# Optimization experiments

Hardware: AMD Instinct MI355X
Metric: run time of the kernel (lower is better)

Reference implementation:

```python
import jax, jax.numpy as jnp
import numpy as np

B, H, W, D = 8, 64, 64, 512
NH, DK = 16, 32
WS, SH = 8, 4            # window size, shift size = WS // 2
L = 4                    # n_layer
WS2 = WS * WS
NWH, NWW = H // WS, W // WS
SCALE = 1.0 / np.sqrt(DK)


def _rel_index(ws):
    # standard Swin relative position index: (ws^2, ws^2) into a (2ws-1)^2 table
    coords = np.stack(np.meshgrid(np.arange(ws), np.arange(ws), indexing='ij'))
    cf = coords.reshape(2, -1)
    rel = cf[:, :, None] - cf[:, None, :] + (ws - 1)
    return (rel[0] * (2 * ws - 1) + rel[1]).astype(np.int32)


def _shift_mask():
    # Swin-style shifted-window attention mask for cyclic shift by SH
    img = np.zeros((H, W), dtype=np.int32)
    cnt = 0
    sls = (slice(0, -WS), slice(-WS, -SH), slice(-SH, None))
    for hs in sls:
        for ws_ in sls:
            img[hs, ws_] = cnt
            cnt += 1
    win = img.reshape(NWH, WS, NWW, WS).transpose(0, 2, 1, 3).reshape(NWH, NWW, WS2)
    m = win[..., None, :] != win[..., :, None]          # (nh, nw, ws2, ws2)
    return np.broadcast_to(m[None, None], (1, NH, NWH, NWW, WS2, WS2)).copy()


def setup_inputs() -> dict:
    key = jax.random.key(0)
    ks = jax.random.split(key, 12)
    s = 0.02
    inp = {
        'x': jax.random.normal(ks[0], (B, H, W, D), jnp.float32),
        'mask': jnp.asarray(_shift_mask()),
        'rel_index': jnp.asarray(_rel_index(WS)),
        'Wq': jax.random.normal(ks[1], (L, D, D), jnp.float32) * s,
        'bq': jnp.zeros((L, D), jnp.float32),
        'Wkv': jax.random.normal(ks[2], (L, D, 2 * D), jnp.float32) * s,
        'bkv': jnp.zeros((L, 2 * D), jnp.float32),
        'Wo': jax.random.normal(ks[3], (L, D, D), jnp.float32) * s,
        'bo': jnp.zeros((L, D), jnp.float32),
        'rel_table': jax.random.normal(ks[4], (L, (2 * WS - 1) ** 2, NH), jnp.float32) * s,
        'ln1_g': jnp.ones((L, D), jnp.float32),
        'ln1_b': jnp.zeros((L, D), jnp.float32),
        'ln2_g': jnp.ones((L, D), jnp.float32),
        'ln2_b': jnp.zeros((L, D), jnp.float32),
        'W1': jax.random.normal(ks[5], (L, D, 4 * D), jnp.float32) * s,
        'b1': jnp.zeros((L, 4 * D), jnp.float32),
        'W2': jax.random.normal(ks[6], (L, 4 * D, D), jnp.float32) * s,
        'b2': jnp.zeros((L, D), jnp.float32),
    }
    return inp


def _ln(x, g, b):
    m = jnp.mean(x, -1, keepdims=True)
    v = jnp.mean(jnp.square(x - m), -1, keepdims=True)
    return (x - m) * jax.lax.rsqrt(v + 1e-5) * g + b


def _partition(t):
    # (B,H,W,NH,DK) -> (B,NH,nh,nw,ws^2,DK)
    t = t.reshape(B, NWH, WS, NWW, WS, NH, DK)
    return t.transpose(0, 5, 1, 3, 2, 4, 6).reshape(B, NH, NWH, NWW, WS2, DK)


def _merge(t):
    # (B,NH,nh,nw,ws^2,DK) -> (B,H,W,NH,DK)
    t = t.reshape(B, NH, NWH, NWW, WS, WS, DK).transpose(0, 2, 4, 3, 5, 1, 6)
    return t.reshape(B, H, W, NH, DK)


def _attn(xn, mask, rel_index, Wq, bq, Wkv, bkv, Wo, bo, table):
    q = (xn @ Wq + bq).reshape(B, H, W, NH, DK)
    kv = (xn @ Wkv + bkv).reshape(B, H, W, 2, NH, DK)
    k, v = kv[..., 0, :, :], kv[..., 1, :, :]
    # cyclic shift (shifting=True since n_class=4)
    q = jnp.roll(q, (-SH, -SH), axis=(1, 2))
    k = jnp.roll(k, (-SH, -SH), axis=(1, 2))
    v = jnp.roll(v, (-SH, -SH), axis=(1, 2))
    qw, kw, vw = _partition(q), _partition(k), _partition(v)
    scores = jnp.einsum('bhnmqd,bhnmkd->bhnmqk', qw, kw) * SCALE
    bias = table[rel_index]                      # (ws2, ws2, NH)
    scores = scores + bias.transpose(2, 0, 1)[None, :, None, None]
    scores = jnp.where(mask, -1e9, scores)
    a = jax.nn.softmax(scores, axis=-1)
    o = jnp.einsum('bhnmqk,bhnmkd->bhnmqd', a, vw)
    o = _merge(o)
    o = jnp.roll(o, (SH, SH), axis=(1, 2))       # reverse cyclic shift
    return o.reshape(B, H, W, D) @ Wo + bo


def reference(x, mask, rel_index, Wq, bq, Wkv, bkv, Wo, bo, rel_table,
              ln1_g, ln1_b, ln2_g, ln2_b, W1, b1, W2, b2):
    for i in range(L):
        x = x + _attn(_ln(x, ln1_g[i], ln1_b[i]), mask, rel_index,
                      Wq[i], bq[i], Wkv[i], bkv[i], Wo[i], bo[i], rel_table[i])
        h = _ln(x, ln2_g[i], ln2_b[i])
        x = x + (jax.nn.gelu(h @ W1[i] + b1[i]) @ W2[i] + b2[i])
    return x
```

## Files before the change

### kernel.cpp

```cpp
#include <hip/hip_runtime.h>
#include <hip/hip_bf16.h>

typedef __hip_bfloat16 bf16;
typedef __attribute__((ext_vector_type(8))) short short8;
typedef __attribute__((ext_vector_type(4))) float f32x4;

#define GLDS16(g, l) __builtin_amdgcn_global_load_lds(                              \
    (__attribute__((address_space(1))) const void*)(g),                             \
    (__attribute__((address_space(3))) void*)(l), 16, 0, 0)

#define SCALE_ 0.17677669529663687f

__global__ void detect_k(const unsigned int* __restrict__ ln1g_raw, int* __restrict__ flag)
{
    if (threadIdx.x == 0) *flag = (ln1g_raw[0] == 0x3F803F80u) ? 0 : 1;
}

__global__ __launch_bounds__(256)
void cvt_small_k(const void* __restrict__ src, bf16* __restrict__ dst, const int n,
                 const int* __restrict__ flag)
{
    const int i = blockIdx.x * 256 + threadIdx.x;
    if (i >= n) return;
    const bool f32 = (*flag != 0);
    dst[i] = f32 ? (bf16)((const float*)src)[i] : ((const bf16*)src)[i];
}

__global__ void transpose2_k(const float* __restrict__ inF, const bf16* __restrict__ inB,
                             bf16* __restrict__ out, const int R, const int C,
                             const int* __restrict__ flag)
{
    __shared__ bf16 tile[32][33];
    const bool f32 = (*flag != 0);
    const int c0 = blockIdx.x * 32, r0 = blockIdx.y * 32;
    const int tx = threadIdx.x, ty = threadIdx.y;
#pragma unroll
    for (int k = 0; k < 4; k++) {
        const long idx = (long)(r0 + ty + k * 8) * C + c0 + tx;
        tile[ty + k * 8][tx] = f32 ? (bf16)inF[idx] : inB[idx];
    }
    __syncthreads();
#pragma unroll
    for (int k = 0; k < 4; k++)
        out[(long)(c0 + ty + k * 8) * R + r0 + tx] = tile[tx][ty + k * 8];
}

__device__ __forceinline__ float gelu_f(float v)
{
    const float u = 0.7978845608028654f * (v + 0.044715f * v * v * v);
    const float e = __expf(-2.0f * u);
    return v * __builtin_amdgcn_rcpf(1.0f + e);
}

#define SBAR()   __builtin_amdgcn_s_barrier()
#define SCHED0() __builtin_amdgcn_sched_barrier(0)
#define WLGKM()  { asm volatile("s_waitcnt lgkmcnt(0)"); SCHED0(); }

template <int EPI>
__global__ __launch_bounds__(512, 2)
void gemm256(const bf16* __restrict__ A, const bf16* __restrict__ Bt,
             const bf16* __restrict__ bias0, const bf16* __restrict__ bias1,
             const int split,
             bf16* __restrict__ outb, float* __restrict__ outf,
             const int M, const int N, const int K)
{
    __shared__ char smem[131072] __attribute__((aligned(16)));

    const int nT  = N >> 8;
    const int nwg = gridDim.x;
    const int bid = blockIdx.x;
    const int wg = (bid & 7) * (nwg >> 3) + (bid >> 3);
    const int mb = wg / nT;
    const int nb = wg - mb * nT;
    const int m0 = mb << 8, n0 = nb << 8;

    const int tid  = threadIdx.x;
    const int lane = tid & 63;
    const int wave = tid >> 6;
    const int wm = wave >> 2;
    const int wn = wave & 3;
    const int fr  = lane & 15;
    const int oct = lane >> 4;
    const int l8  = lane >> 3;
    const int cx  = (lane & 7) ^ l8;

    const int T = K >> 6;

    const bf16* Asrc = A  + (long)(m0 + wm * 128 + wn * 32 + l8) * K + cx * 8;
    char*       Adst = smem + wm * 16384 + wn * 4096;
    const int h    = wn >> 1;
    const int bsub = wm * 2 + (wn & 1);
    const bf16* Bsrc = Bt + (long)(n0 + h * 128 + bsub * 32 + l8) * K + cx * 8;
    char*       Bdst = smem + 65536 + h * 16384 + bsub * 4096;

#define STAGE_A(kt, p) {                                                   \
        const bf16* s_ = Asrc + (long)(kt) * 64;                           \
        char* d_ = Adst + (p) * 32768;                                     \
        GLDS16(s_,            d_);                                         \
        GLDS16(s_ +  8L * K,  d_ + 1024);                                  \
        GLDS16(s_ + 16L * K,  d_ + 2048);                                  \
        GLDS16(s_ + 24L * K,  d_ + 3072); }
#define STAGE_B(kt, p) {                                                   \
        const bf16* s_ = Bsrc + (long)(kt) * 64;                           \
        char* d_ = Bdst + (p) * 32768;                                     \
        GLDS16(s_,            d_);                                         \
        GLDS16(s_ +  8L * K,  d_ + 1024);                                  \
        GLDS16(s_ + 16L * K,  d_ + 2048);                                  \
        GLDS16(s_ + 24L * K,  d_ + 3072); }

    const int kx0 = (     oct * 16) ^ ((fr & 7) << 4);
    const int kx1 = (64 + oct * 16) ^ ((fr & 7) << 4);
    const int aoff = (wm * 128 + fr) * 128;
    const int boff = 65536 + (wn * 64 + fr) * 128;

    f32x4 acc[8][4];
#pragma unroll
    for (int m = 0; m < 8; m++)
#pragma unroll
        for (int n = 0; n < 4; n++) acc[m][n] = (f32x4){0.f, 0.f, 0.f, 0.f};

    short8 af[4][2], bf[4][2];

    STAGE_B(0, 0); STAGE_A(0, 0);
    STAGE_B(1, 1); STAGE_A(1, 1);
    SCHED0();
    asm volatile("s_waitcnt vmcnt(8)");
    SCHED0();
    SBAR();

    for (int t = 0; t < T; ++t) {
        const int pOff = (t & 1) << 15;

#pragma unroll
        for (int mm = 0; mm < 4; mm++) {
            af[mm][0] = *(const short8*)(smem + pOff + aoff + mm * 2048 + kx0);
            af[mm][1] = *(const short8*)(smem + pOff + aoff + mm * 2048 + kx1);
        }
#pragma unroll
        for (int nn = 0; nn < 2; nn++) {
            bf[nn][0] = *(const short8*)(smem + pOff + boff + nn * 2048 + kx0);
            bf[nn][1] = *(const short8*)(smem + pOff + boff + nn * 2048 + kx1);
        }
        SBAR();
        WLGKM();
        __builtin_amdgcn_s_setprio(1);
#pragma unroll
        for (int ks = 0; ks < 2; ks++)
#pragma unroll
            for (int mm = 0; mm < 4; mm++)
#pragma unroll
                for (int nn = 0; nn < 2; nn++)
                    acc[mm][nn] = __builtin_amdgcn_mfma_f32_16x16x32_bf16(
                        bf[nn][ks], af[mm][ks], acc[mm][nn], 0, 0, 0);
        __builtin_amdgcn_s_setprio(0);
        SBAR();

#pragma unroll
        for (int nn = 2; nn < 4; nn++) {
            bf[nn][0] = *(const short8*)(smem + pOff + boff + nn * 2048 + kx0);
            bf[nn][1] = *(const short8*)(smem + pOff + boff + nn * 2048 + kx1);
        }
        SBAR();
        WLGKM();
        __builtin_amdgcn_s_setprio(1);
#pragma unroll
        for (int ks = 0; ks < 2; ks++)
#pragma unroll
            for (int mm = 0; mm < 4; mm++)
#pragma unroll
                for (int nn = 2; nn < 4; nn++)
                    acc[mm][nn] = __builtin_amdgcn_mfma_f32_16x16x32_bf16(
                        bf[nn][ks], af[mm][ks], acc[mm][nn], 0, 0, 0);
        __builtin_amdgcn_s_setprio(0);
        SBAR();

#pragma unroll
        for (int mm = 0; mm < 4; mm++) {
            af[mm][0] = *(const short8*)(smem + pOff + aoff + (4 + mm) * 2048 + kx0);
            af[mm][1] = *(const short8*)(smem + pOff + aoff + (4 + mm) * 2048 + kx1);
        }
        if (t < T - 2) STAGE_B(t + 2, (t & 1));
        SBAR();
        WLGKM();
        __builtin_amdgcn_s_setprio(1);
#pragma unroll
        for (int ks = 0; ks < 2; ks++)
#pragma unroll
            for (int mm = 0; mm < 4; mm++)
#pragma unroll
                for (int nn = 2; nn < 4; nn++)
                    acc[4 + mm][nn] = __builtin_amdgcn_mfma_f32_16x16x32_bf16(
                        bf[nn][ks], af[mm][ks], acc[4 + mm][nn], 0, 0, 0);
        __builtin_amdgcn_s_setprio(0);
        SBAR();

        if (t < T - 2) STAGE_A(t + 2, (t & 1));
        __builtin_amdgcn_s_setprio(1);
#pragma unroll
        for (int ks = 0; ks < 2; ks++)
#pragma unroll
            for (int mm = 0; mm < 4; mm++)
#pragma unroll
                for (int nn = 0; nn < 2; nn++)
                    acc[4 + mm][nn] = __builtin_amdgcn_mfma_f32_16x16x32_bf16(
                        bf[nn][ks], af[mm][ks], acc[4 + mm][nn], 0, 0, 0);
        __builtin_amdgcn_s_setprio(0);
        SCHED0();
        if (t < T - 2)       { asm volatile("s_waitcnt vmcnt(8)"); }
        else if (t == T - 2) { asm volatile("s_waitcnt vmcnt(0)"); }
        SCHED0();
        SBAR();
    }
#undef STAGE_A
#undef STAGE_B

    if (EPI == 2) {
        const int erow = m0 + wm * 128 + fr;
        const int ecol = n0 + wn * 64 + (oct << 2);
#pragma unroll
        for (int nn = 0; nn < 4; nn++) {
            const int col0 = ecol + nn * 16;
            const bf16* bp = (col0 < split) ? (bias0 + col0) : (bias1 + (col0 - split));
            const float bv0 = (float)bp[0], bv1 = (float)bp[1];
            const float bv2 = (float)bp[2], bv3 = (float)bp[3];
#pragma unroll
            for (int mm = 0; mm < 8; mm++) {
                const long base = (long)(erow + mm * 16) * N + col0;
                float4 o = *(const float4*)(outf + base);
                o.x += acc[mm][nn][0] + bv0;
                o.y += acc[mm][nn][1] + bv1;
                o.z += acc[mm][nn][2] + bv2;
                o.w += acc[mm][nn][3] + bv3;
                *(float4*)(outf + base) = o;
            }
        }
    } else {
        const int col_l = wn * 64 + (oct << 2);
#pragma unroll
        for (int nn = 0; nn < 4; nn++) {
            const int cl = col_l + nn * 16;
            const int cg = n0 + cl;
            const bf16* bp = (cg < split) ? (bias0 + cg) : (bias1 + (cg - split));
            const float bv0 = (float)bp[0], bv1 = (float)bp[1];
            const float bv2 = (float)bp[2], bv3 = (float)bp[3];
#pragma unroll
            for (int mm = 0; mm < 8; mm++) {
                const int row_l = wm * 128 + mm * 16 + fr;
                float v0 = acc[mm][nn][0] + bv0;
                float v1 = acc[mm][nn][1] + bv1;
                float v2 = acc[mm][nn][2] + bv2;
                float v3 = acc[mm][nn][3] + bv3;
                if (EPI == 1) { v0 = gelu_f(v0); v1 = gelu_f(v1); v2 = gelu_f(v2); v3 = gelu_f(v3); }
                union { ushort4 u; bf16 hh[4]; } pk;
                pk.hh[0] = (bf16)v0; pk.hh[1] = (bf16)v1;
                pk.hh[2] = (bf16)v2; pk.hh[3] = (bf16)v3;
                int ad = (row_l << 9) + (cl << 1);
                ad ^= ((row_l & 7) << 4);
                *(ushort4*)(smem + ad) = pk.u;
            }
        }
        asm volatile("s_waitcnt lgkmcnt(0)");
        SBAR();
        const int rgrp = tid >> 5;
        const int chnk = tid & 31;
#pragma unroll
        for (int rr = 0; rr < 16; rr++) {
            const int row_l = rgrp * 16 + rr;
            int ad = (row_l << 9) + (chnk << 4);
            ad ^= ((row_l & 7) << 4);
            const uint4 val = *(const uint4*)(smem + ad);
            *(uint4*)((char*)outb + ((long)(m0 + row_l) * N + n0) * 2 + (chnk << 4)) = val;
        }
    }
}

__global__ __launch_bounds__(256)
void ln_k(const float* __restrict__ x, const bf16* __restrict__ g,
          const bf16* __restrict__ b, bf16* __restrict__ out)
{
    const int token = blockIdx.x * 4 + (threadIdx.x >> 6);
    const int lane  = threadIdx.x & 63;
    const float* xp = x + (long)token * 512 + lane * 8;
    float4 u0 = ((const float4*)xp)[0];
    float4 u1 = ((const float4*)xp)[1];
    float v[8] = {u0.x, u0.y, u0.z, u0.w, u1.x, u1.y, u1.z, u1.w};
    float s = 0.f, ss = 0.f;
#pragma unroll
    for (int e = 0; e < 8; e++) { s += v[e]; ss += v[e] * v[e]; }
#pragma unroll
    for (int off = 1; off < 64; off <<= 1) {
        s  += __shfl_xor(s,  off);
        ss += __shfl_xor(ss, off);
    }
    const float mean = s * (1.0f / 512.0f);
    const float var  = ss * (1.0f / 512.0f) - mean * mean;
    const float rstd = rsqrtf(var + 1e-5f);
    union { uint4 u; bf16 h[8]; } gg, bb, oo;
    gg.u = *(const uint4*)(g + lane * 8);
    bb.u = *(const uint4*)(b + lane * 8);
#pragma unroll
    for (int e = 0; e < 8; e++)
        oo.h[e] = (bf16)((v[e] - mean) * rstd * (float)gg.h[e] + (float)bb.h[e]);
    *(uint4*)(out + (long)token * 512 + lane * 8) = oo.u;
}

#define KSTR 36
__global__ __launch_bounds__(64, 2)
void attn_k(const bf16* __restrict__ qkv, const bf16* __restrict__ table,
            bf16* __restrict__ out)
{
    __shared__ float ksm[64 * KSTR];
    __shared__ float vsm[64 * KSTR];
    __shared__ float bias_s[225];

    const int bid = blockIdx.x;
    const int n  = bid & 15;
    const int ww = (bid >> 4) & 7;
    const int wh = (bid >> 7) & 7;
    const int b  = bid >> 10;
    const int i  = threadIdx.x;
    const int ri = i >> 3, ci = i & 7;
    const int gh = (wh * 8 + ri + 4) & 63;
    const int gw = (ww * 8 + ci + 4) & 63;
    const long t = ((long)b * 64 + gh) * 64 + gw;
    const bf16* base = qkv + t * 1536 + n * 32;

    union BU { uint4 u; bf16 h[8]; };

    float q[32];
#pragma unroll
    for (int c = 0; c < 4; c++) {
        BU tu; tu.u = ((const uint4*)base)[c];
#pragma unroll
        for (int e = 0; e < 8; e++) q[c * 8 + e] = (float)tu.h[e];
    }
#pragma unroll
    for (int c = 0; c < 4; c++) {
        BU tu; tu.u = ((const uint4*)(base + 512))[c];
        ((float4*)(ksm + i * KSTR))[c * 2] =
            make_float4((float)tu.h[0], (float)tu.h[1], (float)tu.h[2], (float)tu.h[3]);
        ((float4*)(ksm + i * KSTR))[c * 2 + 1] =
            make_float4((float)tu.h[4], (float)tu.h[5], (float)tu.h[6], (float)tu.h[7]);
    }
#pragma unroll
    for (int c = 0; c < 4; c++) {
        BU tu; tu.u = ((const uint4*)(base + 1024))[c];
        ((float4*)(vsm + i * KSTR))[c * 2] =
            make_float4((float)tu.h[0], (float)tu.h[1], (float)tu.h[2], (float)tu.h[3]);
        ((float4*)(vsm + i * KSTR))[c * 2 + 1] =
            make_float4((float)tu.h[4], (float)tu.h[5], (float)tu.h[6], (float)tu.h[7]);
    }
    for (int idx = i; idx < 225; idx += 64) bias_s[idx] = (float)table[idx * 16 + n];
    __syncthreads();

    const int shi = (wh == 7) ? (ri < 4 ? 1 : 2) : 0;
    const int swi = (ww == 7) ? (ci < 4 ? 1 : 2) : 0;

    float s[64];
#pragma unroll
    for (int j = 0; j < 64; j++) {
        const float4* kr = (const float4*)(ksm + j * KSTR);
        float a0 = 0.f, a1 = 0.f, a2 = 0.f, a3 = 0.f;
#pragma unroll
        for (int c = 0; c < 8; c++) {
            float4 kf = kr[c];
            a0 += q[c * 4 + 0] * kf.x;
            a1 += q[c * 4 + 1] * kf.y;
            a2 += q[c * 4 + 2] * kf.z;
            a3 += q[c * 4 + 3] * kf.w;
        }
        const int rj = j >> 3, cj = j & 7;
        const int shj = (wh == 7) ? (rj < 4 ? 1 : 2) : 0;
        const int swj = (ww == 7) ? (cj < 4 ? 1 : 2) : 0;
        const float bias = bias_s[(ri - rj + 7) * 15 + (ci - cj + 7)];
        const float sc = (a0 + a1 + a2 + a3) * SCALE_ + bias;
        s[j] = ((shj != shi) || (swj != swi)) ? -1.0e9f : sc;
    }
    float m = s[0];
#pragma unroll
    for (int j = 1; j < 64; j++) m = fmaxf(m, s[j]);
    float sum = 0.f;
#pragma unroll
    for (int j = 0; j < 64; j++) { s[j] = __expf(s[j] - m); sum += s[j]; }
    const float inv = 1.0f / sum;

    float o[32];
#pragma unroll
    for (int d = 0; d < 32; d++) o[d] = 0.f;
#pragma unroll
    for (int j = 0; j < 64; j++) {
        const float4* vr = (const float4*)(vsm + j * KSTR);
        const float a = s[j];
#pragma unroll
        for (int c = 0; c < 8; c++) {
            float4 vf = vr[c];
            o[c * 4 + 0] += a * vf.x;
            o[c * 4 + 1] += a * vf.y;
            o[c * 4 + 2] += a * vf.z;
            o[c * 4 + 3] += a * vf.w;
        }
    }
    bf16* op = out + t * 512 + n * 32;
#pragma unroll
    for (int c = 0; c < 4; c++) {
        BU tu;
#pragma unroll
        for (int e = 0; e < 8; e++) tu.h[e] = (bf16)(o[c * 8 + e] * inv);
        ((uint4*)op)[c] = tu.u;
    }
}

__global__ __launch_bounds__(256)
void x2f_k(const void* __restrict__ in, float* __restrict__ out, const long n8,
           const int* __restrict__ flag)
{
    const long idx = (long)blockIdx.x * 256 + threadIdx.x;
    if (idx >= n8) return;
    if (*flag != 0) {
        ((float4*)out)[idx * 2]     = ((const float4*)in)[idx * 2];
        ((float4*)out)[idx * 2 + 1] = ((const float4*)in)[idx * 2 + 1];
    } else {
        union { uint4 u; bf16 h[8]; } t;
        t.u = ((const uint4*)in)[idx];
        ((float4*)out)[idx * 2] =
            make_float4((float)t.h[0], (float)t.h[1], (float)t.h[2], (float)t.h[3]);
        ((float4*)out)[idx * 2 + 1] =
            make_float4((float)t.h[4], (float)t.h[5], (float)t.h[6], (float)t.h[7]);
    }
}

__global__ __launch_bounds__(256)
void copyout_k(const float* __restrict__ in, float* __restrict__ out, const long n8)
{
    const long idx = (long)blockIdx.x * 256 + threadIdx.x;
    if (idx >= n8) return;
    ((float4*)out)[idx * 2]     = ((const float4*)in)[idx * 2];
    ((float4*)out)[idx * 2 + 1] = ((const float4*)in)[idx * 2 + 1];
}

extern "C" void kernel_launch(void* const* d_in, const int* in_sizes, int n_in,
                              void* d_out, int out_size, void* d_ws, size_t ws_size,
                              hipStream_t stream)
{
    const void* x_in = d_in[0];
    const void* Wq   = d_in[3];
    const void* bq   = d_in[4];
    const void* Wkv  = d_in[5];
    const void* bkv  = d_in[6];
    const void* Wo   = d_in[7];
    const void* bo   = d_in[8];
    const void* rtab = d_in[9];
    const void* ln1g = d_in[10];
    const void* ln1b = d_in[11];
    const void* ln2g = d_in[12];
    const void* ln2b = d_in[13];
    const void* W1   = d_in[14];
    const void* b1   = d_in[15];
    const void* W2   = d_in[16];
    const void* b2   = d_in[17];

    if (ws_size < (size_t)260046848) return;

    char* ws = (char*)d_ws;
    float* bufX   = (float*)(ws);
    bf16*  bufXN  = (bf16*)(ws + 67108864);
    bf16*  bufQKV = (bf16*)(ws + 100663296);
    bf16*  bufMLP = bufQKV;
    bf16*  bufATT = (bf16*)(ws + 201326592);
    bf16*  wT     = (bf16*)(ws + 234881024);

    int*  flag = (int*)d_out;
    bf16* pp   = (bf16*)((char*)d_out + 256);
    bf16* p_bq   = pp;
    bf16* p_bkv  = pp + 2048;
    bf16* p_bo   = pp + 6144;
    bf16* p_rtab = pp + 8192;
    bf16* p_l1g  = pp + 22592;
    bf16* p_l1b  = pp + 24640;
    bf16* p_l2g  = pp + 26688;
    bf16* p_l2b  = pp + 28736;
    bf16* p_b1   = pp + 30784;
    bf16* p_b2   = pp + 38976;

    const long LSTR = 3145728;

    detect_k<<<1, 64, 0, stream>>>((const unsigned int*)ln1g, flag);

    cvt_small_k<<<8,  256, 0, stream>>>(bq,   p_bq,   2048,  flag);
    cvt_small_k<<<16, 256, 0, stream>>>(bkv,  p_bkv,  4096,  flag);
    cvt_small_k<<<8,  256, 0, stream>>>(bo,   p_bo,   2048,  flag);
    cvt_small_k<<<57, 256, 0, stream>>>(rtab, p_rtab, 14400, flag);
    cvt_small_k<<<8,  256, 0, stream>>>(ln1g, p_l1g,  2048,  flag);
    cvt_small_k<<<8,  256, 0, stream>>>(ln1b, p_l1b,  2048,  flag);
    cvt_small_k<<<8,  256, 0, stream>>>(ln2g, p_l2g,  2048,  flag);
    cvt_small_k<<<8,  256, 0, stream>>>(ln2b, p_l2b,  2048,  flag);
    cvt_small_k<<<32, 256, 0, stream>>>(b1,   p_b1,   8192,  flag);
    cvt_small_k<<<8,  256, 0, stream>>>(b2,   p_b2,   2048,  flag);

    for (int i = 0; i < 4; i++) {
        bf16* wl = wT + (long)i * LSTR;
        transpose2_k<<<dim3(16,16), dim3(32,8), 0, stream>>>(
            (const float*)Wq  + (long)i*262144,  (const bf16*)Wq  + (long)i*262144,
            wl,           512,  512, flag);
        transpose2_k<<<dim3(32,16), dim3(32,8), 0, stream>>>(
            (const float*)Wkv + (long)i*524288,  (const bf16*)Wkv + (long)i*524288,
            wl + 262144,  512, 1024, flag);
        transpose2_k<<<dim3(16,16), dim3(32,8), 0, stream>>>(
            (const float*)Wo  + (long)i*262144,  (const bf16*)Wo  + (long)i*262144,
            wl + 786432,  512,  512, flag);
        transpose2_k<<<dim3(64,16), dim3(32,8), 0, stream>>>(
            (const float*)W1  + (long)i*1048576, (const bf16*)W1  + (long)i*1048576,
            wl + 1048576, 512, 2048, flag);
        transpose2_k<<<dim3(16,64), dim3(32,8), 0, stream>>>(
            (const float*)W2  + (long)i*1048576, (const bf16*)W2  + (long)i*1048576,
            wl + 2097152, 2048, 512, flag);
    }
    x2f_k<<<8192, 256, 0, stream>>>(x_in, bufX, (long)2097152, flag);

    for (int i = 0; i < 4; i++) {
        const bf16* wl = wT + (long)i * LSTR;
        ln_k<<<8192, 256, 0, stream>>>(bufX, p_l1g + i*512, p_l1b + i*512, bufXN);
        gemm256<0><<<768, 512, 0, stream>>>(bufXN, wl, p_bq + i*512, p_bkv + i*1024, 512,
                                            bufQKV, nullptr, 32768, 1536, 512);
        attn_k<<<8192, 64, 0, stream>>>(bufQKV, p_rtab + i*3600, bufATT);
        gemm256<2><<<256, 512, 0, stream>>>(bufATT, wl + 786432, p_bo + i*512, p_bo + i*512, 512,
                                            nullptr, bufX, 32768, 512, 512);
        ln_k<<<8192, 256, 0, stream>>>(bufX, p_l2g + i*512, p_l2b + i*512, bufXN);
        gemm256<1><<<1024, 512, 0, stream>>>(bufXN, wl + 1048576, p_b1 + i*2048, p_b1 + i*2048, 2048,
                                             bufMLP, nullptr, 32768, 2048, 512);
        gemm256<2><<<256, 512, 0, stream>>>(bufMLP, wl + 2097152, p_b2 + i*512, p_b2 + i*512, 512,
                                            nullptr, bufX, 32768, 512, 2048);
    }
    copyout_k<<<8192, 256, 0, stream>>>(bufX, (float*)d_out, (long)2097152);
}
```

Before: 1.972 ms.

## Rewrite window attention with bf16 MFMA and precomputed bias+mask tables

Replaces the scalar fp32 window-attention kernel with one that computes QK^T and PV using 16x16x32 bf16 MFMA instructions, staging transposed V and softmax probabilities in LDS with an XOR swizzle. Relative-position bias and shift mask are folded into a per-layer precomputed float table indexed by window class and head, removing per-element index math and mask branches. Probabilities are rounded to bf16 before the PV product, which reduces precision, and V is gathered with scalar 2-byte loads.

```diff
diff --git a/kernel.cpp b/kernel.cpp
--- a/kernel.cpp
+++ b/kernel.cpp
@@ -304,109 +304,145 @@
     *(uint4*)(out + (long)token * 512 + lane * 8) = oo.u;
 }
 
-#define KSTR 36
-__global__ __launch_bounds__(64, 2)
-void attn_k(const bf16* __restrict__ qkv, const bf16* __restrict__ table,
-            bf16* __restrict__ out)
-{
-    __shared__ float ksm[64 * KSTR];
-    __shared__ float vsm[64 * KSTR];
-    __shared__ float bias_s[225];
-
+__global__ __launch_bounds__(64)
+void bias_pre_k(const bf16* __restrict__ table, float* __restrict__ biasF)
+{
+    const int blk = blockIdx.x;
+    const int q = blk & 63, n = (blk >> 6) & 15, c = blk >> 10;
+    const int j = threadIdx.x;
+    const int ri = q >> 3, ci = q & 7, rj = j >> 3, cj = j & 7;
+    const float bias = (float)table[((ri - rj + 7) * 15 + (ci - cj + 7)) * 16 + n];
+    const int shi = (c & 1) ? (ri < 4 ? 1 : 2) : 0;
+    const int shj = (c & 1) ? (rj < 4 ? 1 : 2) : 0;
+    const int swi = (c & 2) ? (ci < 4 ? 1 : 2) : 0;
+    const int swj = (c & 2) ? (cj < 4 ? 1 : 2) : 0;
+    biasF[((long)blk << 6) + j] = ((shi != shj) || (swi != swj)) ? -1.0e9f : bias;
+}
+
+__global__ __launch_bounds__(64, 3)
+void attn_k2(const bf16* __restrict__ qkv, const float* __restrict__ biasF,
+             bf16* __restrict__ out)
+{
+    __shared__ char lds[12800];
     const int bid = blockIdx.x;
     const int n  = bid & 15;
     const int ww = (bid >> 4) & 7;
     const int wh = (bid >> 7) & 7;
     const int b  = bid >> 10;
-    const int i  = threadIdx.x;
-    const int ri = i >> 3, ci = i & 7;
-    const int gh = (wh * 8 + ri + 4) & 63;
-    const int gw = (ww * 8 + ci + 4) & 63;
-    const long t = ((long)b * 64 + gh) * 64 + gw;
-    const bf16* base = qkv + t * 1536 + n * 32;
-
-    union BU { uint4 u; bf16 h[8]; };
-
-    float q[32];
-#pragma unroll
-    for (int c = 0; c < 4; c++) {
-        BU tu; tu.u = ((const uint4*)base)[c];
-#pragma unroll
-        for (int e = 0; e < 8; e++) q[c * 8 + e] = (float)tu.h[e];
-    }
-#pragma unroll
-    for (int c = 0; c < 4; c++) {
-        BU tu; tu.u = ((const uint4*)(base + 512))[c];
-        ((float4*)(ksm + i * KSTR))[c * 2] =
-            make_float4((float)tu.h[0], (float)tu.h[1], (float)tu.h[2], (float)tu.h[3]);
-        ((float4*)(ksm + i * KSTR))[c * 2 + 1] =
-            make_float4((float)tu.h[4], (float)tu.h[5], (float)tu.h[6], (float)tu.h[7]);
-    }
-#pragma unroll
-    for (int c = 0; c < 4; c++) {
-        BU tu; tu.u = ((const uint4*)(base + 1024))[c];
-        ((float4*)(vsm + i * KSTR))[c * 2] =
-            make_float4((float)tu.h[0], (float)tu.h[1], (float)tu.h[2], (float)tu.h[3]);
-        ((float4*)(vsm + i * KSTR))[c * 2 + 1] =
-            make_float4((float)tu.h[4], (float)tu.h[5], (float)tu.h[6], (float)tu.h[7]);
-    }
-    for (int idx = i; idx < 225; idx += 64) bias_s[idx] = (float)table[idx * 16 + n];
-    __syncthreads();
-
-    const int shi = (wh == 7) ? (ri < 4 ? 1 : 2) : 0;
-    const int swi = (ww == 7) ? (ci < 4 ? 1 : 2) : 0;
-
-    float s[64];
-#pragma unroll
-    for (int j = 0; j < 64; j++) {
-        const float4* kr = (const float4*)(ksm + j * KSTR);
-        float a0 = 0.f, a1 = 0.f, a2 = 0.f, a3 = 0.f;
-#pragma unroll
-        for (int c = 0; c < 8; c++) {
-            float4 kf = kr[c];
-            a0 += q[c * 4 + 0] * kf.x;
-            a1 += q[c * 4 + 1] * kf.y;
-            a2 += q[c * 4 + 2] * kf.z;
-            a3 += q[c * 4 + 3] * kf.w;
-        }
+    const int lane = threadIdx.x;
+    const int fr  = lane & 15;
+    const int oct = lane >> 4;
+    const int cls = ((wh == 7) ? 1 : 0) | ((ww == 7) ? 2 : 0);
+
+    {
+        const int d  = lane & 31;
+        const int jh = lane >> 5;
+        const long Ce = (((long)b * 64 + wh * 8 + 4) * 64 + (ww * 8 + 4)) * 1536;
+        const long hsub = (wh == 7) ? 6291456L : 0L;
+        const long wsub = (ww == 7) ? 98304L   : 0L;
+        const long vbase = Ce + 1024 + n * 32 + d;
+        long rowb[4];
+#pragma unroll
+        for (int qq = 0; qq < 4; qq++) {
+            const int r = jh * 4 + qq;
+            rowb[qq] = vbase + (long)r * 98304 - (r >= 4 ? hsub : 0);
+        }
+        union { ushort us[8]; uint4 u4; } vg[4];
+#pragma unroll
+        for (int c = 0; c < 32; c++) {
+            const int qq = c >> 3, cj = c & 7;
+            const long a = rowb[qq] + (long)cj * 1536 - (cj >= 4 ? wsub : 0);
+            vg[qq].us[cj] = *(const ushort*)(qkv + a);
+        }
+#pragma unroll
+        for (int qq = 0; qq < 4; qq++)
+            *(uint4*)(lds + d * 144 + jh * 64 + qq * 16) = vg[qq].u4;
+    }
+
+    long tok[4];
+#pragma unroll
+    for (int tt = 0; tt < 4; tt++) {
+        const int j = fr + 16 * tt;
         const int rj = j >> 3, cj = j & 7;
-        const int shj = (wh == 7) ? (rj < 4 ? 1 : 2) : 0;
-        const int swj = (ww == 7) ? (cj < 4 ? 1 : 2) : 0;
-        const float bias = bias_s[(ri - rj + 7) * 15 + (ci - cj + 7)];
-        const float sc = (a0 + a1 + a2 + a3) * SCALE_ + bias;
-        s[j] = ((shj != shi) || (swj != swi)) ? -1.0e9f : sc;
-    }
-    float m = s[0];
-#pragma unroll
-    for (int j = 1; j < 64; j++) m = fmaxf(m, s[j]);
-    float sum = 0.f;
-#pragma unroll
-    for (int j = 0; j < 64; j++) { s[j] = __expf(s[j] - m); sum += s[j]; }
-    const float inv = 1.0f / sum;
-
-    float o[32];
-#pragma unroll
-    for (int d = 0; d < 32; d++) o[d] = 0.f;
-#pragma unroll
-    for (int j = 0; j < 64; j++) {
-        const float4* vr = (const float4*)(vsm + j * KSTR);
-        const float a = s[j];
-#pragma unroll
-        for (int c = 0; c < 8; c++) {
-            float4 vf = vr[c];
-            o[c * 4 + 0] += a * vf.x;
-            o[c * 4 + 1] += a * vf.y;
-            o[c * 4 + 2] += a * vf.z;
-            o[c * 4 + 3] += a * vf.w;
-        }
-    }
-    bf16* op = out + t * 512 + n * 32;
-#pragma unroll
-    for (int c = 0; c < 4; c++) {
-        BU tu;
-#pragma unroll
-        for (int e = 0; e < 8; e++) tu.h[e] = (bf16)(o[c * 8 + e] * inv);
-        ((uint4*)op)[c] = tu.u;
+        const int gh = (wh * 8 + rj + 4) & 63;
+        const int gw = (ww * 8 + cj + 4) & 63;
+        tok[tt] = ((long)b * 64 + gh) * 64 + gw;
+    }
+
+    short8 kf[4];
+#pragma unroll
+    for (int t = 0; t < 4; t++)
+        kf[t] = *(const short8*)(qkv + tok[t] * 1536 + 512 + n * 32 + oct * 8);
+
+    const float* biasW = biasF + (((long)(cls * 16 + n)) << 12);
+    float inv[4];
+#pragma unroll
+    for (int mm = 0; mm < 4; mm++) {
+        const short8 qf = *(const short8*)(qkv + tok[mm] * 1536 + n * 32 + oct * 8);
+        f32x4 sv[4];
+#pragma unroll
+        for (int nn = 0; nn < 4; nn++)
+            sv[nn] = __builtin_amdgcn_mfma_f32_16x16x32_bf16(
+                kf[nn], qf, (f32x4){0.f, 0.f, 0.f, 0.f}, 0, 0, 0);
+        float p[16];
+        float mx = -3.0e38f;
+#pragma unroll
+        for (int nn = 0; nn < 4; nn++) {
+            const f32x4 bz = *(const f32x4*)(biasW + ((fr + 16 * mm) << 6) + nn * 16 + oct * 4);
+#pragma unroll
+            for (int r = 0; r < 4; r++) {
+                p[nn * 4 + r] = sv[nn][r] * SCALE_ + bz[r];
+                mx = fmaxf(mx, p[nn * 4 + r]);
+            }
+        }
+        mx = fmaxf(mx, __shfl_xor(mx, 16));
+        mx = fmaxf(mx, __shfl_xor(mx, 32));
+        float sum = 0.f;
+#pragma unroll
+        for (int e = 0; e < 16; e++) { p[e] = __expf(p[e] - mx); sum += p[e]; }
+        sum += __shfl_xor(sum, 16);
+        sum += __shfl_xor(sum, 32);
+        inv[mm] = __builtin_amdgcn_rcpf(sum);
+
+        const int prow = 4608 + ((fr + 16 * mm) << 7);
+#pragma unroll
+        for (int nn = 0; nn < 4; nn++) {
+            union { bf16 h[2]; unsigned u; } lo, hi;
+            lo.h[0] = (bf16)p[nn * 4 + 0]; lo.h[1] = (bf16)p[nn * 4 + 1];
+            hi.h[0] = (bf16)p[nn * 4 + 2]; hi.h[1] = (bf16)p[nn * 4 + 3];
+            uint2 w; w.x = lo.u; w.y = hi.u;
+            *(uint2*)(lds + prow + ((nn * 32 + oct * 8) ^ ((fr & 7) << 4))) = w;
+        }
+    }
+
+    f32x4 oa[4][2];
+#pragma unroll
+    for (int mm = 0; mm < 4; mm++)
+#pragma unroll
+        for (int nd = 0; nd < 2; nd++) oa[mm][nd] = (f32x4){0.f, 0.f, 0.f, 0.f};
+#pragma unroll
+    for (int kc = 0; kc < 2; kc++) {
+        const short8 vt0 = *(const short8*)(lds + fr * 144        + kc * 64 + oct * 16);
+        const short8 vt1 = *(const short8*)(lds + (fr + 16) * 144 + kc * 64 + oct * 16);
+#pragma unroll
+        for (int mm = 0; mm < 4; mm++) {
+            const short8 pf = *(const short8*)(lds + 4608 + ((fr + 16 * mm) << 7)
+                                  + ((kc * 64 + oct * 16) ^ ((fr & 7) << 4)));
+            oa[mm][0] = __builtin_amdgcn_mfma_f32_16x16x32_bf16(vt0, pf, oa[mm][0], 0, 0, 0);
+            oa[mm][1] = __builtin_amdgcn_mfma_f32_16x16x32_bf16(vt1, pf, oa[mm][1], 0, 0, 0);
+        }
+    }
+
+#pragma unroll
+    for (int mm = 0; mm < 4; mm++) {
+        bf16* op = out + tok[mm] * 512 + n * 32 + oct * 4;
+#pragma unroll
+        for (int nd = 0; nd < 2; nd++) {
+            union { ushort4 u; bf16 h[4]; } o4;
+#pragma unroll
+            for (int r = 0; r < 4; r++) o4.h[r] = (bf16)(oa[mm][nd][r] * inv[mm]);
+            *(ushort4*)(op + nd * 16) = o4.u;
+        }
     }
 }
 
@@ -481,6 +517,7 @@
     bf16* p_l2b  = pp + 28736;
     bf16* p_b1   = pp + 30784;
     bf16* p_b2   = pp + 38976;
+    float* biasAll = (float*)((char*)d_out + 33554432);
 
     const long LSTR = 3145728;
 
@@ -496,6 +533,9 @@
     cvt_small_k<<<8,  256, 0, stream>>>(ln2b, p_l2b,  2048,  flag);
     cvt_small_k<<<32, 256, 0, stream>>>(b1,   p_b1,   8192,  flag);
     cvt_small_k<<<8,  256, 0, stream>>>(b2,   p_b2,   2048,  flag);
+
+    for (int i = 0; i < 4; i++)
+        bias_pre_k<<<4096, 64, 0, stream>>>(p_rtab + i * 3600, biasAll + (long)i * 262144);
 
     for (int i = 0; i < 4; i++) {
         bf16* wl = wT + (long)i * LSTR;
@@ -522,7 +562,7 @@
         ln_k<<<8192, 256, 0, stream>>>(bufX, p_l1g + i*512, p_l1b + i*512, bufXN);
         gemm256<0><<<768, 512, 0, stream>>>(bufXN, wl, p_bq + i*512, p_bkv + i*1024, 512,
                                             bufQKV, nullptr, 32768, 1536, 512);
-        attn_k<<<8192, 64, 0, stream>>>(bufQKV, p_rtab + i*3600, bufATT);
+        attn_k2<<<8192, 64, 0, stream>>>(bufQKV, biasAll + (long)i * 262144, bufATT);
         gemm256<2><<<256, 512, 0, stream>>>(bufATT, wl + 786432, p_bo + i*512, p_bo + i*512, 512,
                                             nullptr, bufX, 32768, 512, 512);
         ln_k<<<8192, 256, 0, stream>>>(bufX, p_l2g + i*512, p_l2b + i*512, bufXN);
```

New measurement: 1.745 ms. -11.5%, faster.
